# Performance work log

Measured on AMD Instinct MI355X. Metric: run time of the kernel, lower is better.

## Reference

```python
import jax, jax.numpy as jnp
import numpy as np

NUM_HEADS = 8
HEAD_DIM = 96
SCALE = HEAD_DIM ** -0.5
STRIDE_Q = (1, 2, 2)
STRIDE_KV = (1, 8, 8)
PAD = [(1, 1), (1, 1), (1, 1)]  # kernel 3 -> padding = 3//2 = 1


def _gelu_pool(t, w, stride, thw):
    """_pre_attention_pool -> GELU -> depthwise Conv3d -> _post_attention_pool.

    t: [B, H, L, hd] flattened tokens; thw = (T, Hs, Ws) with L = T*Hs*Ws.
    Returns pooled [B, H, L', hd] and new thw.
    """
    B, NH, L, C = t.shape
    T, Hs, Ws = thw
    x = t.reshape(B * NH, T, Hs, Ws, C).transpose(0, 4, 1, 2, 3)  # [B*NH, C, T, Hs, Ws]
    x = jax.nn.gelu(x, approximate=False)  # torch F.gelu default (erf)
    x = jax.lax.conv_general_dilated(
        x, w, window_strides=stride, padding=PAD,
        dimension_numbers=('NCDHW', 'OIDHW', 'NCDHW'),
        feature_group_count=C)  # depthwise: groups = head_dim
    new_thw = (x.shape[2], x.shape[3], x.shape[4])
    Lp = new_thw[0] * new_thw[1] * new_thw[2]
    x = x.reshape(B, NH, C, Lp).transpose(0, 1, 3, 2)  # [B, NH, L', C]
    return x, new_thw


def setup_inputs() -> dict:
    key = jax.random.key(0)
    ks = jax.random.split(key, 8)
    B, T, Hs, Ws, C = 2, 8, 56, 56, 768
    L = T * Hs * Ws
    s = 0.02
    return {
        'x': jax.random.normal(ks[0], (B, L, C), jnp.float32),
        'qkv_w': jax.random.normal(ks[1], (3 * C, C), jnp.float32) * s,
        'qkv_b': jnp.zeros((3 * C,), jnp.float32),
        'proj_w': jax.random.normal(ks[2], (C, C), jnp.float32) * s,
        'proj_b': jnp.zeros((C,), jnp.float32),
        'pool_q_w': jax.random.normal(ks[3], (HEAD_DIM, 1, 3, 3, 3), jnp.float32) * 0.1,
        'pool_k_w': jax.random.normal(ks[4], (HEAD_DIM, 1, 3, 3, 3), jnp.float32) * 0.1,
        'pool_v_w': jax.random.normal(ks[5], (HEAD_DIM, 1, 3, 3, 3), jnp.float32) * 0.1,
        't_size': T, 'h_size': Hs, 'w_size': Ws,
    }


def reference(x, qkv_w, qkv_b, proj_w, proj_b, pool_q_w, pool_k_w, pool_v_w,
              t_size, h_size, w_size):
    B, N, C = x.shape
    # fused qkv projection -> [3, B, heads, N, head_dim]
    qkv = (x @ qkv_w.T + qkv_b).reshape(B, N, 3, NUM_HEADS, C // NUM_HEADS)
    qkv = qkv.transpose(2, 0, 3, 1, 4)
    q, k, v = qkv[0], qkv[1], qkv[2]

    thw = (t_size, h_size, w_size)
    q, q_thw = _gelu_pool(q, pool_q_w, STRIDE_Q, thw)
    k, _ = _gelu_pool(k, pool_k_w, STRIDE_KV, thw)
    v, _ = _gelu_pool(v, pool_v_w, STRIDE_KV, thw)

    attn = jax.nn.softmax((q * SCALE) @ jnp.swapaxes(k, -2, -1), axis=-1)
    Nq = q.shape[2]
    out = (attn @ v + q)  # residual_pool=True (iMViT)
    out = out.transpose(0, 2, 1, 3).reshape(B, Nq, C)
    out = out @ proj_w.T + proj_b
    return out
```

## Files before the change

kernel.cpp:

```cpp
#include <hip/hip_runtime.h>
#include <cstdint>

#define NH 8
#define HD 96
#define CDIM 768
#define BQ 2
#define T0 8
#define H0 56
#define W0 56
#define L0 (T0*H0*W0)
#define HP_Q 28
#define WP_Q 28
#define LQ (T0*HP_Q*WP_Q)
#define HP_K 7
#define WP_K 7
#define LK (T0*HP_K*WP_K)
#define LKP 416
#define SCALE 0.10206207261596577f
#define NYC 20
#define MKV 6400
#define NBQ 2352
#define NBKV 600

typedef __bf16 bf16;
typedef bf16 bf16x4 __attribute__((ext_vector_type(4)));
typedef bf16 bf16x8 __attribute__((ext_vector_type(8)));
typedef float f32x4 __attribute__((ext_vector_type(4)));
typedef float f4 __attribute__((ext_vector_type(4)));

#define GPTR(x) ((const __attribute__((address_space(1))) void*)(x))
#define LPTR(x) ((__attribute__((address_space(3))) void*)(x))

__device__ __forceinline__ float fast_gelu(float x) {
    float z = __builtin_fabsf(x) * 0.7071067811865476f;
    float p = 1.f + z*(0.278393f + z*(0.230389f + z*(0.000972f + z*0.078108f)));
    p = p * p;
    p = p * p;
    float e = 1.f - __builtin_amdgcn_rcpf(p);
    float erfv = (x < 0.f) ? -e : e;
    return 0.5f * x * (1.f + erfv);
}

#define NW4 442368
#define NP4 147456
__global__ void cvt_w(const f4* __restrict__ wq, const f4* __restrict__ wp,
                      bf16x4* __restrict__ wqo, bf16x4* __restrict__ wpo) {
    const long total = NW4 + NP4;
    long stride = (long)gridDim.x * blockDim.x;
    for (long i = (long)blockIdx.x * blockDim.x + threadIdx.x; i < total; i += stride) {
        f4 v; bf16x4* o;
        if (i < NW4) { v = wq[i]; o = wqo + i; }
        else         { v = wp[i - NW4]; o = wpo + (i - NW4); }
        bf16x4 t;
        t[0] = (bf16)v[0]; t[1] = (bf16)v[1]; t[2] = (bf16)v[2]; t[3] = (bf16)v[3];
        *o = t;
    }
}

__device__ __forceinline__ int cmap(int i) {
    return ((i + 1) / 3) * 8 + (i + 1) % 3 - 1;
}

__global__ __launch_bounds__(256) void gemm_qkv(
    const float* __restrict__ A, const bf16* __restrict__ Wq,
    const float* __restrict__ bias_q, bf16* __restrict__ OutQ,
    bf16* __restrict__ OutKV)
{
    __shared__ uint8_t sh[2*24576];
    const int tid = threadIdx.x;
    const int lane = tid & 63;
    const int w = tid >> 6;
    const int wr = w >> 1, wc = w & 1;
    const int g = lane >> 4;
    const int ar = lane & 15;
    const int K = 768;

    const int nwg = gridDim.x;
    const int q_ = nwg >> 3, r_ = nwg & 7;
    const int xcd = blockIdx.x & 7, off = blockIdx.x >> 3;
    const int swz = (xcd < r_ ? xcd*(q_+1) : r_*(q_+1) + (xcd - r_)*q_) + off;

    const bool isQ = swz < NBQ;
    const int idx = isQ ? swz : swz - NBQ;
    const int NBN = isQ ? 6 : 12;
    const long bm = idx / NBN, bn = idx % NBN;
    const bf16* B = isQ ? Wq : Wq + (size_t)768*768;
    const float* bias = isQ ? bias_q : bias_q + 768;

    f32x4 acc[4][4];
#pragma unroll
    for (int i = 0; i < 4; ++i)
#pragma unroll
        for (int j = 0; j < 4; ++j) acc[i][j] = (f32x4){0.f,0.f,0.f,0.f};

    const int arow_s = tid >> 3;
    const int csa = (tid & 7) ^ (arow_s & 7);
    long aoff[4];
#pragma unroll
    for (int s = 0; s < 4; ++s) {
        int rA = (int)bm*128 + s*32 + arow_s;
        if (!isQ) {
            int b = rA / 3200; int r = rA - b*3200;
            int t = r / 400;  int rr = r - t*400;
            int yi = rr / NYC, xi = rr - yi*NYC;
            aoff[s] = ((long)b*L0 + (t*H0 + cmap(yi))*W0 + cmap(xi)) * (long)K;
        } else {
            aoff[s] = (long)rA * K;
        }
    }
    const int brow_s = tid >> 2;
    const int csb = (tid & 3) ^ ((tid >> 3) & 3);
    const bf16* Bg = B + (bn*128 + brow_s)*(long)K + csb*8;

    auto stage = [&](int buf, int kt) {
        uint8_t* base = sh + buf*24576;
#pragma unroll
        for (int s = 0; s < 4; ++s)
            __builtin_amdgcn_global_load_lds(GPTR(A + aoff[s] + kt*32 + csa*4),
                LPTR(base + s*4096 + tid*16), 16, 0, 0);
#pragma unroll
        for (int s = 0; s < 2; ++s)
            __builtin_amdgcn_global_load_lds(GPTR(Bg + (long)kt*32 + (long)s*64*K),
                LPTR(base + 16384 + s*4096 + tid*16), 16, 0, 0);
    };
    auto compute = [&](int buf) {
        const float* ldsA = (const float*)(sh + buf*24576);
        const bf16* ldsB = (const bf16*)(sh + buf*24576 + 16384);
        bf16x8 af[4], bfr[4];
#pragma unroll
        for (int i = 0; i < 4; ++i) {
            int R = wr*64 + i*16 + ar;
            f32x4 lo = *(const f32x4*)&ldsA[R*32 + (((2*g    ) ^ (R & 7))*4)];
            f32x4 hi = *(const f32x4*)&ldsA[R*32 + (((2*g + 1) ^ (R & 7))*4)];
            bf16x8 t;
            t[0] = (bf16)lo[0]; t[1] = (bf16)lo[1]; t[2] = (bf16)lo[2]; t[3] = (bf16)lo[3];
            t[4] = (bf16)hi[0]; t[5] = (bf16)hi[1]; t[6] = (bf16)hi[2]; t[7] = (bf16)hi[3];
            af[i] = t;
        }
#pragma unroll
        for (int j = 0; j < 4; ++j) {
            int R = wc*64 + j*16 + ar;
            bfr[j] = *(const bf16x8*)&ldsB[R*32 + ((g ^ ((R >> 1) & 3))*8)];
        }
        __builtin_amdgcn_s_setprio(1);
#pragma unroll
        for (int i = 0; i < 4; ++i)
#pragma unroll
            for (int j = 0; j < 4; ++j)
                acc[i][j] = __builtin_amdgcn_mfma_f32_16x16x32_bf16(af[i], bfr[j], acc[i][j], 0, 0, 0);
        __builtin_amdgcn_s_setprio(0);
    };

    const int nkt = K / 32;
    stage(0, 0);
    for (int kt = 0; kt < nkt; ++kt) {
        const int cur = kt & 1;
        asm volatile("s_waitcnt vmcnt(0)" ::: "memory");
        __builtin_amdgcn_s_barrier();
        __builtin_amdgcn_sched_barrier(0);
        if (kt + 1 < nkt) stage(cur ^ 1, kt + 1);
        compute(cur);
        __builtin_amdgcn_sched_barrier(0);
    }

    __syncthreads();
    bf16* tls = (bf16*)sh;
#pragma unroll
    for (int j = 0; j < 4; ++j) {
        const int colb = (int)bn*128 + wc*64 + j*16;
        const int lcol = wc*64 + j*16 + ar;
        const float bcol = bias[colb + ar];
#pragma unroll
        for (int i = 0; i < 4; ++i) {
            int lrow0 = wr*64 + i*16 + (g << 2);
#pragma unroll
            for (int r = 0; r < 4; ++r)
                tls[(lrow0 + r)*136 + lcol] = (bf16)fast_gelu(acc[i][j][r] + bcol);
        }
    }
    __syncthreads();
#pragma unroll
    for (int it = 0; it < 8; ++it) {
        int idx2 = it*256 + tid;
        int mloc = idx2 >> 4;
        int ck = idx2 & 15;
        bf16x8 v = *(const bf16x8*)&tls[mloc*136 + ck*8];
        int m = (int)bm*128 + mloc;
        int col = (int)bn*128 + ck*8;
        if (isQ) {
            int nh = col / HD;
            int c = col - nh*HD;
            int bflag = m >= L0;
            int l = m - (bflag ? L0 : 0);
            size_t addr = ((size_t)(bflag*8 + nh)*L0 + l)*HD + c;
            *(bf16x8*)&OutQ[addr] = v;
        } else {
            int part = col / 768;
            int cb = col - part*768;
            int nh = cb / HD;
            int c = cb - nh*HD;
            int b = m / 3200; int r = m - b*3200;
            size_t addr = ((size_t)(part*16 + b*8 + nh)*3200 + r)*HD + c;
            *(bf16x8*)&OutKV[addr] = v;
        }
    }
}

__global__ __launch_bounds__(256) void gemm_proj(
    const bf16* __restrict__ A, const bf16* __restrict__ B,
    const float* __restrict__ bias, float* __restrict__ Out,
    int M, int N, int K, int NBN)
{
    __shared__ bf16 sh[2*16384];
    const int tid = threadIdx.x;
    const int lane = tid & 63;
    const int w = tid >> 6;
    const int wr = w >> 1, wc = w & 1;

    const int nwg = gridDim.x;
    const int q_ = nwg >> 3, r_ = nwg & 7;
    const int xcd = blockIdx.x & 7, off = blockIdx.x >> 3;
    const int swz = (xcd < r_ ? xcd*(q_+1) : r_*(q_+1) + (xcd - r_)*q_) + off;
    const long bn = swz % NBN, bm = swz / NBN;

    f32x4 acc[4][4];
#pragma unroll
    for (int i = 0; i < 4; ++i)
#pragma unroll
        for (int j = 0; j < 4; ++j) acc[i][j] = (f32x4){0.f,0.f,0.f,0.f};

    const int trow = tid >> 3;
    const int tchunk = (tid & 7) ^ (trow & 7);
    const bf16* Ag = A + (bm*128 + trow)*(long)K + tchunk*8;
    const bf16* Bg = B + (bn*128 + trow)*(long)K + tchunk*8;

    const int arow = lane & 15;
    const int g8 = (lane >> 4) * 8;
    const int aswz = (arow & 7) * 8;

    auto stage = [&](int buf, int kt) {
        bf16* ldsA = sh + buf*16384;
        bf16* ldsB = sh + buf*16384 + 8192;
#pragma unroll
        for (int s = 0; s < 4; ++s) {
            __builtin_amdgcn_global_load_lds(GPTR(Ag + (long)kt*64 + (long)s*32*K),
                                             LPTR(ldsA + s*2048 + tid*8), 16, 0, 0);
            __builtin_amdgcn_global_load_lds(GPTR(Bg + (long)kt*64 + (long)s*32*K),
                                             LPTR(ldsB + s*2048 + tid*8), 16, 0, 0);
        }
    };
    auto compute = [&](int buf) {
        const bf16* ldsA = sh + buf*16384;
        const bf16* ldsB = sh + buf*16384 + 8192;
#pragma unroll
        for (int kk = 0; kk < 2; ++kk) {
            bf16x8 af[4], bfr[4];
#pragma unroll
            for (int i = 0; i < 4; ++i)
                af[i] = *(const bf16x8*)&ldsA[(wr*64 + i*16 + arow)*64 + ((kk*32 + g8) ^ aswz)];
#pragma unroll
            for (int j = 0; j < 4; ++j)
                bfr[j] = *(const bf16x8*)&ldsB[(wc*64 + j*16 + arow)*64 + ((kk*32 + g8) ^ aswz)];
            __builtin_amdgcn_s_setprio(1);
#pragma unroll
            for (int i = 0; i < 4; ++i)
#pragma unroll
                for (int j = 0; j < 4; ++j)
                    acc[i][j] = __builtin_amdgcn_mfma_f32_16x16x32_bf16(af[i], bfr[j], acc[i][j], 0, 0, 0);
            __builtin_amdgcn_s_setprio(0);
        }
    };

    const int nkt = K / 64;
    stage(0, 0);
    for (int kt = 0; kt < nkt; ++kt) {
        const int cur = kt & 1;
        asm volatile("s_waitcnt vmcnt(0)" ::: "memory");
        __builtin_amdgcn_s_barrier();
        __builtin_amdgcn_sched_barrier(0);
        if (kt + 1 < nkt) stage(cur ^ 1, kt + 1);
        compute(cur);
        __builtin_amdgcn_sched_barrier(0);
    }

#pragma unroll
    for (int j = 0; j < 4; ++j) {
        const int col = (int)bn*128 + wc*64 + j*16 + (lane & 15);
        const float bcol = bias[col];
#pragma unroll
        for (int i = 0; i < 4; ++i) {
            int row0 = (int)bm*128 + wr*64 + i*16 + ((lane>>4)<<2);
#pragma unroll
            for (int r = 0; r < 4; ++r)
                Out[(size_t)(row0 + r)*N + col] = acc[i][j][r] + bcol;
        }
    }
}

__global__ __launch_bounds__(256) void dwconv_all(
    const bf16* __restrict__ qin, const bf16* __restrict__ kv,
    const float* __restrict__ wq, const float* __restrict__ wk,
    const float* __restrict__ wv, bf16* __restrict__ qout,
    bf16* __restrict__ kout, bf16* __restrict__ vtout)
{
    __shared__ float lw[27*HD];
    const int blk = blockIdx.x;
    if (blk < 588) {
        for (int i = threadIdx.x; i < 27*HD; i += 256) {
            int c = i / 27, tap = i % 27;
            lw[tap*HD + c] = wq[i];
        }
        __syncthreads();
        int idx = blk*256 + threadIdx.x;
        if (idx >= 16*HP_Q*WP_Q*12) return;
        int c8 = idx % 12;
        int p = idx / 12;
        int xo = p % WP_Q;
        int yo = (p / WP_Q) % HP_Q;
        int bh = p / (WP_Q*HP_Q);
        const bf16* ip = qin + (size_t)bh * L0 * HD + c8*8;

        float acc[T0][8];
#pragma unroll
        for (int t = 0; t < T0; ++t)
#pragma unroll
            for (int j = 0; j < 8; ++j) acc[t][j] = 0.f;

#pragma unroll
        for (int dy = 0; dy < 3; ++dy) {
            int y = yo*2 + dy - 1;
            if ((unsigned)y >= (unsigned)H0) continue;
#pragma unroll
            for (int dx = 0; dx < 3; ++dx) {
                int x = xo*2 + dx - 1;
                if ((unsigned)x >= (unsigned)W0) continue;
                float wreg[3][8];
#pragma unroll
                for (int dt = 0; dt < 3; ++dt)
#pragma unroll
                    for (int j = 0; j < 8; ++j)
                        wreg[dt][j] = lw[(dt*9 + dy*3 + dx)*HD + c8*8 + j];
                const bf16* colp = ip + ((size_t)(y*W0 + x))*HD;
#pragma unroll
                for (int t = 0; t < T0; ++t) {
                    bf16x8 v = *(const bf16x8*)(colp + (size_t)t*H0*W0*HD);
                    float f[8];
#pragma unroll
                    for (int j = 0; j < 8; ++j) f[j] = (float)v[j];
#pragma unroll
                    for (int dt = 0; dt < 3; ++dt) {
                        int to = t - dt + 1;
                        if (to < 0 || to >= T0) continue;
#pragma unroll
                        for (int j = 0; j < 8; ++j)
                            acc[to][j] += wreg[dt][j] * f[j];
                    }
                }
            }
        }

#pragma unroll
        for (int to = 0; to < T0; ++to) {
            int l = (to*HP_Q + yo)*WP_Q + xo;
            bf16x8 ov;
#pragma unroll
            for (int j = 0; j < 8; ++j) ov[j] = (bf16)acc[to][j];
            *(bf16x8*)&qout[((size_t)bh*LQ + l)*HD + c8*8] = ov;
        }
        return;
    }

    const int kb = blk - 588;
    const int seg = kb / 40;
    const int lb  = kb % 40;
    const float* w = seg ? wv : wk;
    const bf16* in = kv + (size_t)seg * 16 * 3200 * HD;
    for (int i = threadIdx.x; i < 27*HD; i += 256) {
        int c = i / 27, tap = i % 27;
        lw[tap*HD + c] = w[i];
    }
    __syncthreads();

    if (lb >= 37) {
        int pid = (lb - 37)*256 + threadIdx.x;
        if (seg == 0) {
            for (int e = pid; e < 16*24*96; e += 768) {
                int bh = e / (24*96); int rem = e - bh*24*96;
                int l = LK + rem / 96; int c = rem % 96;
                kout[((size_t)bh*LKP + l)*HD + c] = (bf16)0.f;
            }
        } else {
            for (int e = pid; e < 16*96*24; e += 768) {
                int bh = e / (96*24); int rem = e - bh*96*24;
                int c = rem / 24; int l = LK + rem % 24;
                vtout[((size_t)bh*HD + c)*LKP + l] = (bf16)0.f;
            }
        }
        return;
    }

    int idx = lb*256 + threadIdx.x;
    if (idx >= 16*HP_K*WP_K*12) return;
    int c8 = idx % 12;
    int p = idx / 12;
    int xo = p % WP_K;
    int yo = (p / WP_K) % HP_K;
    int bh = p / (WP_K*HP_K);
    const bf16* ip = in + (size_t)bh * 3200 * HD + c8*8;

    float acc[T0][8];
#pragma unroll
    for (int t = 0; t < T0; ++t)
#pragma unroll
        for (int j = 0; j < 8; ++j) acc[t][j] = 0.f;

#pragma unroll
    for (int dy = 0; dy < 3; ++dy) {
        int yi = 3*yo + dy - 1;
        if ((unsigned)yi >= (unsigned)NYC) continue;
#pragma unroll
        for (int dx = 0; dx < 3; ++dx) {
            int xi = 3*xo + dx - 1;
            if ((unsigned)xi >= (unsigned)NYC) continue;
            float wreg[3][8];
#pragma unroll
            for (int dt = 0; dt < 3; ++dt)
#pragma unroll
                for (int j = 0; j < 8; ++j)
                    wreg[dt][j] = lw[(dt*9 + dy*3 + dx)*HD + c8*8 + j];
            const bf16* colp = ip + ((size_t)(yi*NYC + xi))*HD;
#pragma unroll
            for (int t = 0; t < T0; ++t) {
                bf16x8 v = *(const bf16x8*)(colp + (size_t)t*400*HD);
                float f[8];
#pragma unroll
                for (int j = 0; j < 8; ++j) f[j] = (float)v[j];
#pragma unroll
                for (int dt = 0; dt < 3; ++dt) {
                    int to = t - dt + 1;
                    if (to < 0 || to >= T0) continue;
#pragma unroll
                    for (int j = 0; j < 8; ++j)
                        acc[to][j] += wreg[dt][j] * f[j];
                }
            }
        }
    }

#pragma unroll
    for (int to = 0; to < T0; ++to) {
        int l = (to*HP_K + yo)*WP_K + xo;
        if (seg == 1) {
#pragma unroll
            for (int j = 0; j < 8; ++j)
                vtout[((size_t)bh*HD + c8*8 + j)*LKP + l] = (bf16)acc[to][j];
        } else {
            bf16x8 ov;
#pragma unroll
            for (int j = 0; j < 8; ++j) ov[j] = (bf16)acc[to][j];
            *(bf16x8*)&kout[((size_t)bh*LKP + l)*HD + c8*8] = ov;
        }
    }
}

__global__ __launch_bounds__(256) void attn_mfma(
    const bf16* __restrict__ q, const bf16* __restrict__ k,
    const bf16* __restrict__ vt, bf16* __restrict__ out)
{
    const int tid = threadIdx.x;
    const int lane = tid & 63;
    const int w = tid >> 6;
    const int col = lane & 15;
    const int g = lane >> 4;
    const int blk = blockIdx.x;
    const int qblk = blk % (LQ/64);
    const int bh = blk / (LQ/64);
    const int q0 = qblk*64 + w*16;

    const bf16* Qp  = q  + ((size_t)bh*LQ + q0)*HD;
    const bf16* Kp  = k  + (size_t)bh*LKP*HD;
    const bf16* VTp = vt + (size_t)bh*HD*LKP;

    bf16x8 qf[3];
#pragma unroll
    for (int c = 0; c < 3; ++c)
        qf[c] = *(const bf16x8*)&Qp[(size_t)col*HD + c*32 + g*8];

    f32x4 o[6];
#pragma unroll
    for (int t = 0; t < 6; ++t) o[t] = (f32x4){0.f,0.f,0.f,0.f};
    float lsum = 0.f;

    for (int kc = 0; kc < LKP/32; ++kc) {
        const int kvb = kc*32;
        uint32_t P[2][2];
#pragma unroll
        for (int s = 0; s < 2; ++s) {
            f32x4 acc = (f32x4){0.f,0.f,0.f,0.f};
#pragma unroll
            for (int c = 0; c < 3; ++c) {
                bf16x8 kf = *(const bf16x8*)&Kp[(size_t)(kvb + s*16 + col)*HD + c*32 + g*8];
                acc = __builtin_amdgcn_mfma_f32_16x16x32_bf16(kf, qf[c], acc, 0, 0, 0);
            }
            bf16x4 pb;
#pragma unroll
            for (int r = 0; r < 4; ++r) {
                int kv = kvb + s*16 + g*4 + r;
                float p = (kv < LK) ? __expf(acc[r]*SCALE) : 0.f;
                lsum += p;
                pb[r] = (bf16)p;
            }
            union { bf16x4 v; uint32_t u[2]; } pk; pk.v = pb;
            P[s][0] = pk.u[0]; P[s][1] = pk.u[1];
        }
        uint32_t sa0 = (g < 2) ? P[1][0] : P[0][0];
        uint32_t sa1 = (g < 2) ? P[1][1] : P[0][1];
        uint32_t tb0 = (g < 2) ? P[0][0] : P[1][0];
        uint32_t tb1 = (g < 2) ? P[0][1] : P[1][1];
        uint32_t R32_0 = (uint32_t)__shfl_xor((int)sa0, 32);
        uint32_t R32_1 = (uint32_t)__shfl_xor((int)sa1, 32);
        uint32_t R48_0 = (uint32_t)__shfl_xor((int)sa0, 48);
        uint32_t R48_1 = (uint32_t)__shfl_xor((int)sa1, 48);
        uint32_t R16_0 = (uint32_t)__shfl_xor((int)tb0, 16);
        uint32_t R16_1 = (uint32_t)__shfl_xor((int)tb1, 16);
        union { uint32_t u[4]; bf16x8 v; } pf;
        pf.u[0] = (g == 0) ? P[0][0] : (g == 1) ? R48_0 : (g == 2) ? R32_0 : R16_0;
        pf.u[1] = (g == 0) ? P[0][1] : (g == 1) ? R48_1 : (g == 2) ? R32_1 : R16_1;
        pf.u[2] = (g == 0) ? R16_0 : (g == 1) ? R32_0 : (g == 2) ? R48_0 : P[1][0];
        pf.u[3] = (g == 0) ? R16_1 : (g == 1) ? R32_1 : (g == 2) ? R48_1 : P[1][1];
#pragma unroll
        for (int t = 0; t < 6; ++t) {
            bf16x8 vf = *(const bf16x8*)&VTp[(size_t)(t*16 + col)*LKP + kvb + g*8];
            o[t] = __builtin_amdgcn_mfma_f32_16x16x32_bf16(vf, pf.v, o[t], 0, 0, 0);
        }
    }

    lsum += __shfl_xor(lsum, 16);
    lsum += __shfl_xor(lsum, 32);
    float inv = 1.f / lsum;

    const int b = bh >> 3, nh = bh & 7;
    size_t obase = ((size_t)b*LQ + q0 + col)*CDIM + (size_t)nh*HD;
#pragma unroll
    for (int t = 0; t < 6; ++t) {
        bf16x4 qres = *(const bf16x4*)&Qp[(size_t)col*HD + t*16 + g*4];
        bf16x4 ov;
#pragma unroll
        for (int r = 0; r < 4; ++r)
            ov[r] = (bf16)(o[t][r]*inv + (float)qres[r]);
        *(bf16x4*)&out[obase + t*16 + g*4] = ov;
    }
}

extern "C" void kernel_launch(void* const* d_in, const int* in_sizes, int n_in,
                              void* d_out, int out_size, void* d_ws, size_t ws_size,
                              hipStream_t stream) {
    const float* x      = (const float*)d_in[0];
    const float* qkv_w  = (const float*)d_in[1];
    const float* qkv_b  = (const float*)d_in[2];
    const float* proj_w = (const float*)d_in[3];
    const float* proj_b = (const float*)d_in[4];
    const float* pq_w   = (const float*)d_in[5];
    const float* pk_w   = (const float*)d_in[6];
    const float* pv_w   = (const float*)d_in[7];

    uint8_t* ws = (uint8_t*)d_ws;
    bf16* qg_out   = (bf16*)(ws);
    bf16* kv_c     = (bf16*)(ws +  77070336);
    bf16* wqkv_bf  = (bf16*)(ws +  96731136);
    bf16* wproj_bf = (bf16*)(ws + 100270080);
    bf16* q_bf     = (bf16*)(ws + 101449728);
    bf16* k_bf     = (bf16*)(ws + 120717312);
    bf16* vt_bf    = (bf16*)(ws + 121995264);
    bf16* attn_o   = (bf16*)(ws + 123273216);

    cvt_w<<<576, 256, 0, stream>>>((const f4*)qkv_w, (const f4*)proj_w,
                                   (bf16x4*)wqkv_bf, (bf16x4*)wproj_bf);

    gemm_qkv<<<NBQ + NBKV, 256, 0, stream>>>(x, wqkv_bf, qkv_b, qg_out, kv_c);

    dwconv_all<<<668, 256, 0, stream>>>(qg_out, kv_c, pq_w, pk_w, pv_w,
                                        q_bf, k_bf, vt_bf);

    attn_mfma<<<16*(LQ/64), 256, 0, stream>>>(q_bf, k_bf, vt_bf, attn_o);

    gemm_proj<<<6*98, 256, 0, stream>>>(
        attn_o, wproj_bf, proj_b, (float*)d_out, 12544, 768, 768, 6);
}
```

Measured before the change: 301.2 us.

## Convert QKV A-tile to bf16 in registers and prefetch next tile before waiting

The QKV GEMM now loads fp32 A tiles into registers, converts them to bf16 and writes them to LDS itself, instead of async-copying fp32 into LDS and converting on every fragment read. This shrinks the LDS footprint and removes repeated conversions in the compute loop. Both GEMMs now issue the next stage's global loads before waiting with a partial vmcnt, so loads overlap compute. A second barrier is added per iteration to protect buffer reuse, which adds sync cost.

```diff
diff --git a/kernel.cpp b/kernel.cpp
--- a/kernel.cpp
+++ b/kernel.cpp
@@ -66,7 +66,7 @@
     const float* __restrict__ bias_q, bf16* __restrict__ OutQ,
     bf16* __restrict__ OutKV)
 {
-    __shared__ uint8_t sh[2*24576];
+    __shared__ uint8_t sh[34816];
     const int tid = threadIdx.x;
     const int lane = tid & 63;
     const int w = tid >> 6;
@@ -94,7 +94,9 @@
         for (int j = 0; j < 4; ++j) acc[i][j] = (f32x4){0.f,0.f,0.f,0.f};
 
     const int arow_s = tid >> 3;
-    const int csa = (tid & 7) ^ (arow_s & 7);
+    const int qa = tid & 7;
+    const int swA = (arow_s >> 1) & 3;
+    const int qsA = ((qa >> 1) ^ swA) * 2 + (qa & 1);
     long aoff[4];
 #pragma unroll
     for (int s = 0; s < 4; ++s) {
@@ -112,30 +114,36 @@
     const int csb = (tid & 3) ^ ((tid >> 3) & 3);
     const bf16* Bg = B + (bn*128 + brow_s)*(long)K + csb*8;
 
-    auto stage = [&](int buf, int kt) {
-        uint8_t* base = sh + buf*24576;
+    f32x4 rN[4];
+    auto loadA = [&](int kt) {
 #pragma unroll
         for (int s = 0; s < 4; ++s)
-            __builtin_amdgcn_global_load_lds(GPTR(A + aoff[s] + kt*32 + csa*4),
-                LPTR(base + s*4096 + tid*16), 16, 0, 0);
+            rN[s] = *(const f32x4*)(A + aoff[s] + kt*32 + qsA*4);
+    };
+    auto writeA = [&](int buf) {
+        bf16* ldsA = (bf16*)(sh + buf*16384);
+#pragma unroll
+        for (int s = 0; s < 4; ++s) {
+            bf16x4 t;
+            t[0] = (bf16)rN[s][0]; t[1] = (bf16)rN[s][1];
+            t[2] = (bf16)rN[s][2]; t[3] = (bf16)rN[s][3];
+            *(bf16x4*)&ldsA[(s*32 + arow_s)*32 + qa*4] = t;
+        }
+    };
+    auto gloadB = [&](int buf, int kt) {
 #pragma unroll
         for (int s = 0; s < 2; ++s)
             __builtin_amdgcn_global_load_lds(GPTR(Bg + (long)kt*32 + (long)s*64*K),
-                LPTR(base + 16384 + s*4096 + tid*16), 16, 0, 0);
+                LPTR(sh + buf*16384 + 8192 + s*4096 + tid*16), 16, 0, 0);
     };
     auto compute = [&](int buf) {
-        const float* ldsA = (const float*)(sh + buf*24576);
-        const bf16* ldsB = (const bf16*)(sh + buf*24576 + 16384);
+        const bf16* ldsA = (const bf16*)(sh + buf*16384);
+        const bf16* ldsB = (const bf16*)(sh + buf*16384 + 8192);
         bf16x8 af[4], bfr[4];
 #pragma unroll
         for (int i = 0; i < 4; ++i) {
             int R = wr*64 + i*16 + ar;
-            f32x4 lo = *(const f32x4*)&ldsA[R*32 + (((2*g    ) ^ (R & 7))*4)];
-            f32x4 hi = *(const f32x4*)&ldsA[R*32 + (((2*g + 1) ^ (R & 7))*4)];
-            bf16x8 t;
-            t[0] = (bf16)lo[0]; t[1] = (bf16)lo[1]; t[2] = (bf16)lo[2]; t[3] = (bf16)lo[3];
-            t[4] = (bf16)hi[0]; t[5] = (bf16)hi[1]; t[6] = (bf16)hi[2]; t[7] = (bf16)hi[3];
-            af[i] = t;
+            af[i] = *(const bf16x8*)&ldsA[R*32 + ((g ^ ((R >> 1) & 3))*8)];
         }
 #pragma unroll
         for (int j = 0; j < 4; ++j) {
@@ -152,15 +160,26 @@
     };
 
     const int nkt = K / 32;
-    stage(0, 0);
+    loadA(0);
+    gloadB(0, 0);
+    writeA(0);
     for (int kt = 0; kt < nkt; ++kt) {
-        const int cur = kt & 1;
-        asm volatile("s_waitcnt vmcnt(0)" ::: "memory");
+        const int cur = kt & 1, nxt = cur ^ 1;
+        const bool pre = (kt + 1 < nkt);
+        if (pre) {
+            loadA(kt + 1);
+            gloadB(nxt, kt + 1);
+            asm volatile("s_waitcnt vmcnt(6)" ::: "memory");
+        } else {
+            asm volatile("s_waitcnt vmcnt(0)" ::: "memory");
+        }
+        asm volatile("s_waitcnt lgkmcnt(0)" ::: "memory");
         __builtin_amdgcn_s_barrier();
         __builtin_amdgcn_sched_barrier(0);
-        if (kt + 1 < nkt) stage(cur ^ 1, kt + 1);
         compute(cur);
+        if (pre) writeA(nxt);
         __builtin_amdgcn_sched_barrier(0);
+        __builtin_amdgcn_s_barrier();
     }
 
     __syncthreads();
@@ -274,13 +293,17 @@
     const int nkt = K / 64;
     stage(0, 0);
     for (int kt = 0; kt < nkt; ++kt) {
-        const int cur = kt & 1;
-        asm volatile("s_waitcnt vmcnt(0)" ::: "memory");
+        if (kt + 1 < nkt) {
+            stage((kt + 1) & 1, kt + 1);
+            asm volatile("s_waitcnt vmcnt(8)" ::: "memory");
+        } else {
+            asm volatile("s_waitcnt vmcnt(0)" ::: "memory");
+        }
         __builtin_amdgcn_s_barrier();
         __builtin_amdgcn_sched_barrier(0);
-        if (kt + 1 < nkt) stage(cur ^ 1, kt + 1);
-        compute(cur);
+        compute(kt & 1);
         __builtin_amdgcn_sched_barrier(0);
+        __builtin_amdgcn_s_barrier();
     }
 
 #pragma unroll
```

Result: faster. 294.2 us (-2.3%).

## Pre-convert activations to bf16 and restructure QKV GEMM pipeline with BK=64

Applied to the files above, without the earlier changes.

Adds a conversion pass that turns the fp32 input activations into bf16 before the QKV GEMM, so the GEMM loads bf16 tiles directly into LDS with a K-step of 64 instead of loading fp32 and converting in registers. The prefetch of the next stage is moved ahead of the wait, using a partial vmcnt wait plus an extra barrier, in both GEMM kernels. This removes per-tile conversion work and halves the A-tile bytes read by the GEMM. In exchange it adds a full read and write of the activation tensor in the conversion kernel, plus a larger workspace.

```diff
diff --git a/kernel.cpp b/kernel.cpp
--- a/kernel.cpp
+++ b/kernel.cpp
@@ -41,16 +41,19 @@
     return 0.5f * x * (1.f + erfv);
 }
 
+#define NX4 9633792
 #define NW4 442368
 #define NP4 147456
-__global__ void cvt_w(const f4* __restrict__ wq, const f4* __restrict__ wp,
-                      bf16x4* __restrict__ wqo, bf16x4* __restrict__ wpo) {
-    const long total = NW4 + NP4;
+__global__ void cvt_all(const f4* __restrict__ x, const f4* __restrict__ wq,
+                        const f4* __restrict__ wp, bf16x4* __restrict__ xo,
+                        bf16x4* __restrict__ wqo, bf16x4* __restrict__ wpo) {
+    const long total = (long)NX4 + NW4 + NP4;
     long stride = (long)gridDim.x * blockDim.x;
     for (long i = (long)blockIdx.x * blockDim.x + threadIdx.x; i < total; i += stride) {
         f4 v; bf16x4* o;
-        if (i < NW4) { v = wq[i]; o = wqo + i; }
-        else         { v = wp[i - NW4]; o = wpo + (i - NW4); }
+        if (i < NX4)            { v = x[i];              o = xo + i; }
+        else if (i < NX4 + NW4) { v = wq[i - NX4];       o = wqo + (i - NX4); }
+        else                    { v = wp[i - NX4 - NW4]; o = wpo + (i - NX4 - NW4); }
         bf16x4 t;
         t[0] = (bf16)v[0]; t[1] = (bf16)v[1]; t[2] = (bf16)v[2]; t[3] = (bf16)v[3];
         *o = t;
@@ -62,17 +65,15 @@
 }
 
 __global__ __launch_bounds__(256) void gemm_qkv(
-    const float* __restrict__ A, const bf16* __restrict__ Wq,
+    const bf16* __restrict__ A, const bf16* __restrict__ Wq,
     const float* __restrict__ bias_q, bf16* __restrict__ OutQ,
     bf16* __restrict__ OutKV)
 {
-    __shared__ uint8_t sh[2*24576];
+    __shared__ bf16 sh[2*16384];
     const int tid = threadIdx.x;
     const int lane = tid & 63;
     const int w = tid >> 6;
     const int wr = w >> 1, wc = w & 1;
-    const int g = lane >> 4;
-    const int ar = lane & 15;
     const int K = 768;
 
     const int nwg = gridDim.x;
@@ -93,12 +94,13 @@
 #pragma unroll
         for (int j = 0; j < 4; ++j) acc[i][j] = (f32x4){0.f,0.f,0.f,0.f};
 
-    const int arow_s = tid >> 3;
-    const int csa = (tid & 7) ^ (arow_s & 7);
+    const int trow = tid >> 3;
+    const int tchunk = (tid & 7) ^ (trow & 7);
+
     long aoff[4];
 #pragma unroll
     for (int s = 0; s < 4; ++s) {
-        int rA = (int)bm*128 + s*32 + arow_s;
+        int rA = (int)bm*128 + s*32 + trow;
         if (!isQ) {
             int b = rA / 3200; int r = rA - b*3200;
             int t = r / 400;  int rr = r - t*400;
@@ -108,71 +110,71 @@
             aoff[s] = (long)rA * K;
         }
     }
-    const int brow_s = tid >> 2;
-    const int csb = (tid & 3) ^ ((tid >> 3) & 3);
-    const bf16* Bg = B + (bn*128 + brow_s)*(long)K + csb*8;
+    const bf16* Bg = B + (bn*128 + trow)*(long)K + tchunk*8;
+
+    const int arow = lane & 15;
+    const int g8 = (lane >> 4) * 8;
+    const int aswz = (arow & 7) * 8;
 
     auto stage = [&](int buf, int kt) {
-        uint8_t* base = sh + buf*24576;
-#pragma unroll
-        for (int s = 0; s < 4; ++s)
-            __builtin_amdgcn_global_load_lds(GPTR(A + aoff[s] + kt*32 + csa*4),
-                LPTR(base + s*4096 + tid*16), 16, 0, 0);
-#pragma unroll
-        for (int s = 0; s < 2; ++s)
-            __builtin_amdgcn_global_load_lds(GPTR(Bg + (long)kt*32 + (long)s*64*K),
-                LPTR(base + 16384 + s*4096 + tid*16), 16, 0, 0);
+        bf16* ldsA = sh + buf*16384;
+        bf16* ldsB = sh + buf*16384 + 8192;
+#pragma unroll
+        for (int s = 0; s < 4; ++s) {
+            __builtin_amdgcn_global_load_lds(GPTR(A + aoff[s] + kt*64 + tchunk*8),
+                                             LPTR(ldsA + s*2048 + tid*8), 16, 0, 0);
+            __builtin_amdgcn_global_load_lds(GPTR(Bg + (long)kt*64 + (long)s*32*K),
+                                             LPTR(ldsB + s*2048 + tid*8), 16, 0, 0);
+        }
     };
     auto compute = [&](int buf) {
-        const float* ldsA = (const float*)(sh + buf*24576);
-        const bf16* ldsB = (const bf16*)(sh + buf*24576 + 16384);
-        bf16x8 af[4], bfr[4];
-#pragma unroll
-        for (int i = 0; i < 4; ++i) {
-            int R = wr*64 + i*16 + ar;
-            f32x4 lo = *(const f32x4*)&ldsA[R*32 + (((2*g    ) ^ (R & 7))*4)];
-            f32x4 hi = *(const f32x4*)&ldsA[R*32 + (((2*g + 1) ^ (R & 7))*4)];
-            bf16x8 t;
-            t[0] = (bf16)lo[0]; t[1] = (bf16)lo[1]; t[2] = (bf16)lo[2]; t[3] = (bf16)lo[3];
-            t[4] = (bf16)hi[0]; t[5] = (bf16)hi[1]; t[6] = (bf16)hi[2]; t[7] = (bf16)hi[3];
-            af[i] = t;
-        }
-#pragma unroll
-        for (int j = 0; j < 4; ++j) {
-            int R = wc*64 + j*16 + ar;
-            bfr[j] = *(const bf16x8*)&ldsB[R*32 + ((g ^ ((R >> 1) & 3))*8)];
-        }
-        __builtin_amdgcn_s_setprio(1);
-#pragma unroll
-        for (int i = 0; i < 4; ++i)
+        const bf16* ldsA = sh + buf*16384;
+        const bf16* ldsB = sh + buf*16384 + 8192;
+#pragma unroll
+        for (int kk = 0; kk < 2; ++kk) {
+            bf16x8 af[4], bfr[4];
+#pragma unroll
+            for (int i = 0; i < 4; ++i)
+                af[i] = *(const bf16x8*)&ldsA[(wr*64 + i*16 + arow)*64 + ((kk*32 + g8) ^ aswz)];
 #pragma unroll
             for (int j = 0; j < 4; ++j)
-                acc[i][j] = __builtin_amdgcn_mfma_f32_16x16x32_bf16(af[i], bfr[j], acc[i][j], 0, 0, 0);
-        __builtin_amdgcn_s_setprio(0);
+                bfr[j] = *(const bf16x8*)&ldsB[(wc*64 + j*16 + arow)*64 + ((kk*32 + g8) ^ aswz)];
+            __builtin_amdgcn_s_setprio(1);
+#pragma unroll
+            for (int i = 0; i < 4; ++i)
+#pragma unroll
+                for (int j = 0; j < 4; ++j)
+                    acc[i][j] = __builtin_amdgcn_mfma_f32_16x16x32_bf16(af[i], bfr[j], acc[i][j], 0, 0, 0);
+            __builtin_amdgcn_s_setprio(0);
+        }
     };
 
-    const int nkt = K / 32;
+    const int nkt = K / 64;
     stage(0, 0);
     for (int kt = 0; kt < nkt; ++kt) {
-        const int cur = kt & 1;
-        asm volatile("s_waitcnt vmcnt(0)" ::: "memory");
+        if (kt + 1 < nkt) {
+            stage((kt + 1) & 1, kt + 1);
+            asm volatile("s_waitcnt vmcnt(8)" ::: "memory");
+        } else {
+            asm volatile("s_waitcnt vmcnt(0)" ::: "memory");
+        }
         __builtin_amdgcn_s_barrier();
         __builtin_amdgcn_sched_barrier(0);
-        if (kt + 1 < nkt) stage(cur ^ 1, kt + 1);
-        compute(cur);
+        compute(kt & 1);
         __builtin_amdgcn_sched_barrier(0);
+        __builtin_amdgcn_s_barrier();
     }
 
     __syncthreads();
-    bf16* tls = (bf16*)sh;
+    bf16* tls = sh;
 #pragma unroll
     for (int j = 0; j < 4; ++j) {
         const int colb = (int)bn*128 + wc*64 + j*16;
-        const int lcol = wc*64 + j*16 + ar;
-        const float bcol = bias[colb + ar];
+        const int lcol = wc*64 + j*16 + (lane & 15);
+        const float bcol = bias[colb + (lane & 15)];
 #pragma unroll
         for (int i = 0; i < 4; ++i) {
-            int lrow0 = wr*64 + i*16 + (g << 2);
+            int lrow0 = wr*64 + i*16 + ((lane>>4)<<2);
 #pragma unroll
             for (int r = 0; r < 4; ++r)
                 tls[(lrow0 + r)*136 + lcol] = (bf16)fast_gelu(acc[i][j][r] + bcol);
@@ -274,13 +276,17 @@
     const int nkt = K / 64;
     stage(0, 0);
     for (int kt = 0; kt < nkt; ++kt) {
-        const int cur = kt & 1;
-        asm volatile("s_waitcnt vmcnt(0)" ::: "memory");
+        if (kt + 1 < nkt) {
+            stage((kt + 1) & 1, kt + 1);
+            asm volatile("s_waitcnt vmcnt(8)" ::: "memory");
+        } else {
+            asm volatile("s_waitcnt vmcnt(0)" ::: "memory");
+        }
         __builtin_amdgcn_s_barrier();
         __builtin_amdgcn_sched_barrier(0);
-        if (kt + 1 < nkt) stage(cur ^ 1, kt + 1);
-        compute(cur);
+        compute(kt & 1);
         __builtin_amdgcn_sched_barrier(0);
+        __builtin_amdgcn_s_barrier();
     }
 
 #pragma unroll
@@ -565,19 +571,20 @@
     const float* pv_w   = (const float*)d_in[7];
 
     uint8_t* ws = (uint8_t*)d_ws;
-    bf16* qg_out   = (bf16*)(ws);
-    bf16* kv_c     = (bf16*)(ws +  77070336);
-    bf16* wqkv_bf  = (bf16*)(ws +  96731136);
-    bf16* wproj_bf = (bf16*)(ws + 100270080);
-    bf16* q_bf     = (bf16*)(ws + 101449728);
-    bf16* k_bf     = (bf16*)(ws + 120717312);
-    bf16* vt_bf    = (bf16*)(ws + 121995264);
-    bf16* attn_o   = (bf16*)(ws + 123273216);
-
-    cvt_w<<<576, 256, 0, stream>>>((const f4*)qkv_w, (const f4*)proj_w,
-                                   (bf16x4*)wqkv_bf, (bf16x4*)wproj_bf);
-
-    gemm_qkv<<<NBQ + NBKV, 256, 0, stream>>>(x, wqkv_bf, qkv_b, qg_out, kv_c);
+    bf16* x_bf     = (bf16*)(ws);
+    bf16* qg_out   = (bf16*)(ws +  77070336);
+    bf16* kv_c     = (bf16*)(ws + 154140672);
+    bf16* wqkv_bf  = (bf16*)(ws + 173801472);
+    bf16* wproj_bf = (bf16*)(ws + 177340416);
+    bf16* q_bf     = (bf16*)(ws + 178520064);
+    bf16* k_bf     = (bf16*)(ws + 197787648);
+    bf16* vt_bf    = (bf16*)(ws + 199065600);
+    bf16* attn_o   = (bf16*)(ws + 200343552);
+
+    cvt_all<<<2560, 256, 0, stream>>>((const f4*)x, (const f4*)qkv_w, (const f4*)proj_w,
+                                      (bf16x4*)x_bf, (bf16x4*)wqkv_bf, (bf16x4*)wproj_bf);
+
+    gemm_qkv<<<NBQ + NBKV, 256, 0, stream>>>(x_bf, wqkv_bf, qkv_b, qg_out, kv_c);
 
     dwconv_all<<<668, 256, 0, stream>>>(qg_out, kv_c, pq_w, pk_w, pv_w,
                                         q_bf, k_bf, vt_bf);
```

Result: faster. 283.5 us (median of 3 runs) (-5.9%).
